# Kernel tuning notes

Hardware: AMD Instinct MI355X
Metric: run time of the kernel (lower is better)

## Reference

```python
import jax, jax.numpy as jnp
import numpy as np

HIDDEN = 512
HEADS = 8
HEAD_DIM = HIDDEN // HEADS


def setup_inputs() -> dict:
    key = jax.random.key(0)
    ks = jax.random.split(key, 12)
    B, S = 2, 2048
    s = 1.0 / np.sqrt(HIDDEN)
    inp = {
        "query": jax.random.normal(ks[0], (B, S, HIDDEN), dtype=jnp.float32),
        "key": jax.random.normal(ks[1], (B, S, HIDDEN), dtype=jnp.float32),
        "value": jax.random.normal(ks[2], (B, S, HIDDEN), dtype=jnp.float32),
        "Wq": jax.random.uniform(ks[3], (HIDDEN, HIDDEN), jnp.float32, -s, s),
        "bq": jnp.zeros((HIDDEN,), jnp.float32),
        "Wk": jax.random.uniform(ks[4], (HIDDEN, HIDDEN), jnp.float32, -s, s),
        "bk": jnp.zeros((HIDDEN,), jnp.float32),
        "Wv": jax.random.uniform(ks[5], (HIDDEN, HIDDEN), jnp.float32, -s, s),
        "bv": jnp.zeros((HIDDEN,), jnp.float32),
        "Wo": jax.random.uniform(ks[6], (HIDDEN, HIDDEN), jnp.float32, -s, s),
        "bo": jnp.zeros((HIDDEN,), jnp.float32),
    }
    return inp


def reference(query, key, value, Wq, bq, Wk, bk, Wv, bv, Wo, bo):
    B, S, _ = query.shape
    scale = jnp.sqrt(jnp.asarray(HEAD_DIM, dtype=query.dtype))
    # Linear projections (torch Linear: x @ W.T + b)
    Q = (query @ Wq.T + bq).reshape(B, S, HEADS, HEAD_DIM).transpose(0, 2, 1, 3)
    K = (key @ Wk.T + bk).reshape(B, S, HEADS, HEAD_DIM).transpose(0, 2, 1, 3)
    V = (value @ Wv.T + bv).reshape(B, S, HEADS, HEAD_DIM).transpose(0, 2, 1, 3)
    # Scores: [B, H, S, S]
    energy = jnp.einsum("bhqd,bhkd->bhqk", Q, K) / scale
    attn = jax.nn.softmax(energy, axis=-1)
    # Dropout is identity in eval mode.
    x = jnp.einsum("bhqk,bhkd->bhqd", attn, V)
    x = x.transpose(0, 2, 1, 3).reshape(B, S, HIDDEN)
    return x @ Wo.T + bo
```

## Files before the change

kernel.cpp:

```cpp
#include <hip/hip_runtime.h>

typedef __bf16 bf16x8 __attribute__((ext_vector_type(8)));
typedef float f32x4 __attribute__((ext_vector_type(4)));
typedef unsigned int uint4v __attribute__((ext_vector_type(4)));
typedef unsigned int uint2v __attribute__((ext_vector_type(2)));

__device__ __forceinline__ unsigned short f2bf(float f) {
  union { float f; unsigned int u; } v; v.f = f;
  unsigned int u = v.u;
  u += 0x7FFFu + ((u >> 16) & 1u);
  return (unsigned short)(u >> 16);
}

__device__ __forceinline__ unsigned int pack2bf(float a, float b) {
  return (unsigned int)f2bf(a) | ((unsigned int)f2bf(b) << 16);
}

__device__ __forceinline__ unsigned int packtrunc(float a, float b) {
  return __builtin_amdgcn_perm(__float_as_uint(b), __float_as_uint(a),
                               0x07060302u);
}

__device__ __forceinline__ bf16x8 as_bf(uint4v u) {
  union { uint4v u; bf16x8 b; } c; c.u = u; return c.b;
}

__global__ __launch_bounds__(256) void convert_w(
    const float* wq, const float* wk, const float* wv, const float* wo,
    unsigned short* wqc, unsigned short* wkc, unsigned short* wvc,
    unsigned short* woc, float qscale)
{
  const float* src; unsigned short* dst; float sc = 1.f;
  switch (blockIdx.y) {
    case 0: src = wq; dst = wqc; sc = qscale; break;
    case 1: src = wk; dst = wkc; break;
    case 2: src = wv; dst = wvc; break;
    default: src = wo; dst = woc; break;
  }
  int idx = (blockIdx.x * 256 + threadIdx.x) * 8;
  f32x4 a = *(const f32x4*)(src + idx);
  f32x4 b = *(const f32x4*)(src + idx + 4);
  uint4v p;
  p.x = pack2bf(a.x * sc, a.y * sc);
  p.y = pack2bf(a.z * sc, a.w * sc);
  p.z = pack2bf(b.x * sc, b.y * sc);
  p.w = pack2bf(b.z * sc, b.w * sc);
  *(uint4v*)(dst + idx) = p;
}

template<int OUT, bool AF32>
__device__ __forceinline__ void gemm_core(
    const void* __restrict__ Ap, const unsigned short* __restrict__ W,
    const float* __restrict__ bias, void* __restrict__ Cp,
    float bscale, int mbase, int nbase)
{
  __shared__ union {
    struct { unsigned short As[2][64][40]; unsigned short Bs[2][128][40]; } t;
    unsigned short Cs[128][72];
  } u;

  const int tid  = threadIdx.x;
  const int wave = tid >> 6, lane = tid & 63;
  const int lrow = lane & 15, lgrp = lane >> 4;
  const int ar = tid >> 2, ac = (tid & 3) * 8;

  const unsigned short* Bg0 = W + (size_t)(nbase + ar) * 512 + ac;
  const unsigned short* Bg1 = W + (size_t)(nbase + ar + 64) * 512 + ac;

  f32x4 acc[4][2];
#pragma unroll
  for (int i = 0; i < 4; i++)
#pragma unroll
    for (int j = 0; j < 2; j++) acc[i][j] = (f32x4){0.f, 0.f, 0.f, 0.f};

  const unsigned short* Ab = (const unsigned short*)Ap;
  const float*          Af = (const float*)Ap;
  uint4v pA; f32x4 pAf0, pAf1;
  if constexpr (AF32) {
    const float* base = Af + (size_t)(mbase + ar) * 512 + ac;
    pAf0 = *(const f32x4*)(base);
    pAf1 = *(const f32x4*)(base + 4);
  } else {
    pA = *(const uint4v*)(Ab + (size_t)(mbase + ar) * 512 + ac);
  }
  uint4v pB0 = *(const uint4v*)Bg0;
  uint4v pB1 = *(const uint4v*)Bg1;

  for (int kt = 0; kt < 512; kt += 32) {
    const int buf = (kt >> 5) & 1;
    if constexpr (AF32) {
      uint4v w;
      w.x = pack2bf(pAf0.x, pAf0.y); w.y = pack2bf(pAf0.z, pAf0.w);
      w.z = pack2bf(pAf1.x, pAf1.y); w.w = pack2bf(pAf1.z, pAf1.w);
      *(uint4v*)&u.t.As[buf][ar][ac] = w;
    } else {
      *(uint4v*)&u.t.As[buf][ar][ac] = pA;
    }
    *(uint4v*)&u.t.Bs[buf][ar][ac]      = pB0;
    *(uint4v*)&u.t.Bs[buf][ar + 64][ac] = pB1;
    if (kt + 32 < 512) {
      if constexpr (AF32) {
        const float* base = Af + (size_t)(mbase + ar) * 512 + ac + kt + 32;
        pAf0 = *(const f32x4*)(base);
        pAf1 = *(const f32x4*)(base + 4);
      } else {
        pA = *(const uint4v*)(Ab + (size_t)(mbase + ar) * 512 + ac + kt + 32);
      }
      pB0 = *(const uint4v*)(Bg0 + kt + 32);
      pB1 = *(const uint4v*)(Bg1 + kt + 32);
    }
    __syncthreads();
    bf16x8 a[4], b[2];
#pragma unroll
    for (int mi = 0; mi < 4; mi++)
      a[mi] = *(const bf16x8*)&u.t.As[buf][mi * 16 + lrow][lgrp * 8];
#pragma unroll
    for (int ni = 0; ni < 2; ni++)
      b[ni] = *(const bf16x8*)&u.t.Bs[buf][wave * 32 + ni * 16 + lrow][lgrp * 8];
#pragma unroll
    for (int mi = 0; mi < 4; mi++)
#pragma unroll
      for (int ni = 0; ni < 2; ni++)
        acc[mi][ni] = __builtin_amdgcn_mfma_f32_16x16x32_bf16(
            a[mi], b[ni], acc[mi][ni], 0, 0, 0);
  }

  if constexpr (OUT == 2) {
    __syncthreads();
#pragma unroll
    for (int ni = 0; ni < 2; ni++) {
      int col_l = wave * 32 + ni * 16 + lrow;
      float bv = bias[nbase + col_l];
#pragma unroll
      for (int mi = 0; mi < 4; mi++) {
        int row_l = mi * 16 + lgrp * 4;
#pragma unroll
        for (int r = 0; r < 4; r++)
          u.Cs[col_l][row_l + r] = f2bf(acc[mi][ni][r] + bv);
      }
    }
    __syncthreads();
    const int bb = mbase >> 11, s_base = mbase & 2047;
    unsigned short* Vt = (unsigned short*)Cp;
#pragma unroll
    for (int ks = 0; ks < 4; ks++) {
      int seg = tid + ks * 256;
      int c = seg >> 3, r0 = (seg & 7) * 8;
      uint4v val = *(const uint4v*)&u.Cs[c][r0];
      int n = nbase + c, hh = n >> 6, d = n & 63;
      int sr = s_base + r0;
      int P0 = (sr & ~31) | (((sr >> 3) & 1) << 4) | (((sr >> 4) & 1) << 2);
      unsigned short* dst = Vt + ((size_t)(bb * 8 + hh) * 64 + d) * 2048;
      *(uint2v*)(dst + P0)     = (uint2v){val.x, val.y};
      *(uint2v*)(dst + P0 + 8) = (uint2v){val.z, val.w};
    }
  } else {
#pragma unroll
    for (int ni = 0; ni < 2; ni++) {
      int col = nbase + wave * 32 + ni * 16 + lrow;
      float bv = bias[col] * bscale;
#pragma unroll
      for (int mi = 0; mi < 4; mi++) {
        int row0 = mbase + mi * 16 + lgrp * 4;
#pragma unroll
        for (int r = 0; r < 4; r++) {
          float val = acc[mi][ni][r] + bv;
          if constexpr (OUT == 0)
            ((unsigned short*)Cp)[(size_t)(row0 + r) * 512 + col] = f2bf(val);
          else
            ((float*)Cp)[(size_t)(row0 + r) * 512 + col] = val;
        }
      }
    }
  }
}

__global__ __launch_bounds__(256) void qkv_gemm(
    const float* q, const float* k, const float* v,
    const unsigned short* wqc, const unsigned short* wkc,
    const unsigned short* wvc,
    const float* bq, const float* bk, const float* bv,
    unsigned short* Qb, unsigned short* Kb, unsigned short* Vt, float qscale)
{
  const int z = blockIdx.z;
  const int mb = blockIdx.y * 64, nb = blockIdx.x * 128;
  if (z == 2)      gemm_core<2, true>(v, wvc, bv, Vt, 1.f, mb, nb);
  else if (z == 0) gemm_core<0, true>(q, wqc, bq, Qb, qscale, mb, nb);
  else             gemm_core<0, true>(k, wkc, bk, Kb, 1.f, mb, nb);
}

__global__ __launch_bounds__(256) void out_gemm(
    const unsigned short* ctx, const unsigned short* woc,
    const float* bo, float* out)
{
  __shared__ unsigned short As[2][64][40];
  __shared__ unsigned short Bs[2][64][40];

  const int tid  = threadIdx.x;
  const int wave = tid >> 6, lane = tid & 63;
  const int lrow = lane & 15, lgrp = lane >> 4;
  const int mbase = blockIdx.y * 64, nbase = blockIdx.x * 64;
  const int ar = tid >> 2, ac = (tid & 3) * 8;

  const unsigned short* Ag = ctx + (size_t)(mbase + ar) * 512 + ac;
  const unsigned short* Bg = woc + (size_t)(nbase + ar) * 512 + ac;

  f32x4 acc[4];
#pragma unroll
  for (int i = 0; i < 4; i++) acc[i] = (f32x4){0.f, 0.f, 0.f, 0.f};

  uint4v pA = *(const uint4v*)Ag;
  uint4v pB = *(const uint4v*)Bg;

  for (int kt = 0; kt < 512; kt += 32) {
    const int buf = (kt >> 5) & 1;
    *(uint4v*)&As[buf][ar][ac] = pA;
    *(uint4v*)&Bs[buf][ar][ac] = pB;
    if (kt + 32 < 512) {
      pA = *(const uint4v*)(Ag + kt + 32);
      pB = *(const uint4v*)(Bg + kt + 32);
    }
    __syncthreads();
    bf16x8 a[4];
#pragma unroll
    for (int mi = 0; mi < 4; mi++)
      a[mi] = *(const bf16x8*)&As[buf][mi * 16 + lrow][lgrp * 8];
    bf16x8 b = *(const bf16x8*)&Bs[buf][wave * 16 + lrow][lgrp * 8];
#pragma unroll
    for (int mi = 0; mi < 4; mi++)
      acc[mi] = __builtin_amdgcn_mfma_f32_16x16x32_bf16(a[mi], b, acc[mi], 0, 0, 0);
  }

  int col = nbase + wave * 16 + lrow;
  float bv = bo[col];
#pragma unroll
  for (int mi = 0; mi < 4; mi++) {
    int row0 = mbase + mi * 16 + lgrp * 4;
#pragma unroll
    for (int r = 0; r < 4; r++)
      out[(size_t)(row0 + r) * 512 + col] = acc[mi][r] + bv;
  }
}

__global__ __launch_bounds__(256, 3) void attn_kernel(
    const unsigned short* Qb, const unsigned short* Kb,
    const unsigned short* Vt, unsigned short* ctx)
{
  __shared__ unsigned short Ks[128][74];
  __shared__ unsigned short Vs[64][134];

  const int tid  = threadIdx.x;
  const int wave = tid >> 6, lane = tid & 63;
  const int lrow = lane & 15, lgrp = lane >> 4;
  const int qh = wave >> 1, kh = wave & 1;
  const int bh = blockIdx.y, b = bh >> 3, h = bh & 7;
  const int qbase = blockIdx.x * 64;

  const unsigned short* Qg  = Qb + (size_t)(b * 2048 + qbase) * 512 + h * 64;
  const unsigned short* Kg  = Kb + (size_t)(b * 2048) * 512 + h * 64;
  const unsigned short* Vtg = Vt + (size_t)bh * 64 * 2048;

#pragma unroll
  for (int i = 0; i < 2; i++) {
    int seg = tid + i * 256;
    int row = seg >> 3, c0 = (seg & 7) * 8;
    *(uint4v*)&Vs[row][c0] = *(const uint4v*)(Qg + (size_t)row * 512 + c0);
  }
  __syncthreads();
  bf16x8 qf[2][2];
#pragma unroll
  for (int qt = 0; qt < 2; qt++)
#pragma unroll
    for (int ks = 0; ks < 2; ks++)
      qf[qt][ks] = *(const bf16x8*)&Vs[qh * 32 + qt * 16 + lrow][ks * 32 + lgrp * 8];

  bf16x8 vone;
  { uint4v o = (uint4v){0x3F803F80u, 0x3F803F80u, 0x3F803F80u, 0x3F803F80u};
    vone = as_bf(o); }

  const int s0  = tid >> 3, kc_ = (tid & 7) * 8;
  const int vd0 = tid >> 4, vc_ = (tid & 15) * 8;

  f32x4 oacc[2][5];
#pragma unroll
  for (int qt = 0; qt < 2; qt++)
#pragma unroll
    for (int d = 0; d < 5; d++) oacc[qt][d] = (f32x4){0.f, 0.f, 0.f, 0.f};

  uint4v kr[4], vr[4];
#pragma unroll
  for (int i = 0; i < 4; i++) {
    kr[i] = *(const uint4v*)(Kg + (size_t)(s0 + 32 * i) * 512 + kc_);
    vr[i] = *(const uint4v*)(Vtg + (size_t)(vd0 + 16 * i) * 2048 + vc_);
  }
  __syncthreads();

  for (int it = 0; it < 16; ++it) {
#pragma unroll
    for (int i = 0; i < 4; i++) {
      *(uint4v*)&Ks[s0 + 32 * i][kc_]  = kr[i];
      *(uint4v*)&Vs[vd0 + 16 * i][vc_] = vr[i];
    }
    __syncthreads();
    if (it < 15) {
      const int key0 = (it + 1) * 128;
#pragma unroll
      for (int i = 0; i < 4; i++) {
        kr[i] = *(const uint4v*)(Kg + (size_t)(key0 + s0 + 32 * i) * 512 + kc_);
        vr[i] = *(const uint4v*)(Vtg + (size_t)(vd0 + 16 * i) * 2048 + key0 + vc_);
      }
    }

    f32x4 sacc[2][4];
#pragma unroll
    for (int qt = 0; qt < 2; qt++)
#pragma unroll
      for (int kt = 0; kt < 4; kt++) sacc[qt][kt] = (f32x4){0.f, 0.f, 0.f, 0.f};
#pragma unroll
    for (int kt = 0; kt < 4; kt++) {
      bf16x8 a0 = *(const bf16x8*)&Ks[kh * 64 + kt * 16 + lrow][lgrp * 8];
      bf16x8 a1 = *(const bf16x8*)&Ks[kh * 64 + kt * 16 + lrow][32 + lgrp * 8];
#pragma unroll
      for (int qt = 0; qt < 2; qt++) {
        sacc[qt][kt] = __builtin_amdgcn_mfma_f32_16x16x32_bf16(a0, qf[qt][0], sacc[qt][kt], 0, 0, 0);
        sacc[qt][kt] = __builtin_amdgcn_mfma_f32_16x16x32_bf16(a1, qf[qt][1], sacc[qt][kt], 0, 0, 0);
      }
    }

#pragma unroll
    for (int qt = 0; qt < 2; qt++)
#pragma unroll
      for (int kt = 0; kt < 4; kt++)
#pragma unroll
        for (int r = 0; r < 4; r++)
          sacc[qt][kt][r] = __builtin_amdgcn_exp2f(sacc[qt][kt][r]);

#pragma unroll
    for (int c = 0; c < 2; c++) {
      bf16x8 pf[2];
#pragma unroll
      for (int qt = 0; qt < 2; qt++) {
        uint4v pk;
        pk.x = packtrunc(sacc[qt][2 * c][0],     sacc[qt][2 * c][1]);
        pk.y = packtrunc(sacc[qt][2 * c][2],     sacc[qt][2 * c][3]);
        pk.z = packtrunc(sacc[qt][2 * c + 1][0], sacc[qt][2 * c + 1][1]);
        pk.w = packtrunc(sacc[qt][2 * c + 1][2], sacc[qt][2 * c + 1][3]);
        pf[qt] = as_bf(pk);
      }
#pragma unroll
      for (int dt = 0; dt < 5; dt++) {
        bf16x8 vb = (dt < 4)
          ? *(const bf16x8*)&Vs[dt * 16 + lrow][(2 * kh + c) * 32 + lgrp * 8]
          : vone;
#pragma unroll
        for (int qt = 0; qt < 2; qt++)
          oacc[qt][dt] = __builtin_amdgcn_mfma_f32_16x16x32_bf16(vb, pf[qt], oacc[qt][dt], 0, 0, 0);
      }
    }
    __syncthreads();
  }

  float* Obuf = (float*)&Ks[0][0];
  float* Lbuf = Obuf + 64 * 68;
  if (kh == 1) {
#pragma unroll
    for (int qt = 0; qt < 2; qt++) {
      int qrow = qh * 32 + qt * 16 + lrow;
#pragma unroll
      for (int dt = 0; dt < 4; dt++)
#pragma unroll
        for (int r = 0; r < 4; r++)
          Obuf[qrow * 68 + dt * 16 + lgrp * 4 + r] = oacc[qt][dt][r];
      if (lgrp == 0) Lbuf[qrow] = oacc[qt][4][0];
    }
  }
  __syncthreads();
  if (kh == 0) {
#pragma unroll
    for (int qt = 0; qt < 2; qt++) {
      int qrow = qh * 32 + qt * 16 + lrow;
      float inv = 1.0f / (oacc[qt][4][0] + Lbuf[qrow]);
#pragma unroll
      for (int dt = 0; dt < 4; dt++)
#pragma unroll
        for (int r = 0; r < 4; r++) {
          float val = (oacc[qt][dt][r] + Obuf[qrow * 68 + dt * 16 + lgrp * 4 + r]) * inv;
          Vs[qrow][dt * 16 + lgrp * 4 + r] = f2bf(val);
        }
    }
  }
  __syncthreads();
  unsigned short* Cg = ctx + (size_t)(b * 2048 + qbase) * 512 + h * 64;
#pragma unroll
  for (int i = 0; i < 2; i++) {
    int seg = tid + i * 256;
    int row = seg >> 3, c0 = (seg & 7) * 8;
    *(uint4v*)(Cg + (size_t)row * 512 + c0) = *(const uint4v*)&Vs[row][c0];
  }
}

extern "C" void kernel_launch(void* const* d_in, const int* in_sizes, int n_in,
                              void* d_out, int out_size, void* d_ws, size_t ws_size,
                              hipStream_t stream)
{
  const float* q  = (const float*)d_in[0];
  const float* k  = (const float*)d_in[1];
  const float* v  = (const float*)d_in[2];
  const float* Wq = (const float*)d_in[3];
  const float* bq = (const float*)d_in[4];
  const float* Wk = (const float*)d_in[5];
  const float* bk = (const float*)d_in[6];
  const float* Wv = (const float*)d_in[7];
  const float* bv = (const float*)d_in[8];
  const float* Wo = (const float*)d_in[9];
  const float* bo = (const float*)d_in[10];
  float* out = (float*)d_out;

  unsigned short* wqc = (unsigned short*)d_ws;
  unsigned short* wkc = wqc + (1 << 18);
  unsigned short* wvc = wkc + (1 << 18);
  unsigned short* woc = wvc + (1 << 18);
  unsigned short* Qb  = woc + (1 << 18);
  unsigned short* Kb  = Qb  + (1 << 21);
  unsigned short* Vt  = Kb  + (1 << 21);
  unsigned short* Cb  = Vt  + (1 << 21);

  const float qscale = 0.125f * 1.44269504088896340736f;

  convert_w<<<dim3(128, 4), 256, 0, stream>>>(
      Wq, Wk, Wv, Wo, wqc, wkc, wvc, woc, qscale);
  qkv_gemm<<<dim3(4, 64, 3), 256, 0, stream>>>(
      q, k, v, wqc, wkc, wvc, bq, bk, bv, Qb, Kb, Vt, qscale);
  attn_kernel<<<dim3(32, 16), 256, 0, stream>>>(Qb, Kb, Vt, Cb);
  out_gemm<<<dim3(8, 64), 256, 0, stream>>>(Cb, woc, bo, out);
}
```

Measured before the change: 144.9 us.

## Widen attention block to 128 queries with 8 waves sharing K/V tiles

The attention kernel now uses 512 threads per block covering 128 query rows instead of 64, so each K/V tile staged in shared memory is reused by twice as many waves and the grid halves. Each thread loads half as many K/V segments per iteration. The shared buffers become a union with a larger fp32 merge area, and the final normalized context is written straight to global memory as packed bf16 pairs instead of going through a shared-memory staging pass. The cost is fewer blocks (256) and lower occupancy bounds, plus narrower, less coalesced output stores.

```diff
diff --git a/kernel.cpp b/kernel.cpp
--- a/kernel.cpp
+++ b/kernel.cpp
@@ -242,19 +242,21 @@
   }
 }
 
-__global__ __launch_bounds__(256, 3) void attn_kernel(
+__global__ __launch_bounds__(512, 2) void attn_kernel(
     const unsigned short* Qb, const unsigned short* Kb,
     const unsigned short* Vt, unsigned short* ctx)
 {
-  __shared__ unsigned short Ks[128][74];
-  __shared__ unsigned short Vs[64][134];
+  __shared__ union {
+    struct { unsigned short Ks[128][74]; unsigned short Vs[64][134]; } s;
+    struct { float O[128][68]; float L[128]; } m;
+  } u;
 
   const int tid  = threadIdx.x;
   const int wave = tid >> 6, lane = tid & 63;
   const int lrow = lane & 15, lgrp = lane >> 4;
   const int qh = wave >> 1, kh = wave & 1;
   const int bh = blockIdx.y, b = bh >> 3, h = bh & 7;
-  const int qbase = blockIdx.x * 64;
+  const int qbase = blockIdx.x * 128;
 
   const unsigned short* Qg  = Qb + (size_t)(b * 2048 + qbase) * 512 + h * 64;
   const unsigned short* Kg  = Kb + (size_t)(b * 2048) * 512 + h * 64;
@@ -262,9 +264,9 @@
 
 #pragma unroll
   for (int i = 0; i < 2; i++) {
-    int seg = tid + i * 256;
+    int seg = tid + i * 512;
     int row = seg >> 3, c0 = (seg & 7) * 8;
-    *(uint4v*)&Vs[row][c0] = *(const uint4v*)(Qg + (size_t)row * 512 + c0);
+    *(uint4v*)&u.s.Ks[row][c0] = *(const uint4v*)(Qg + (size_t)row * 512 + c0);
   }
   __syncthreads();
   bf16x8 qf[2][2];
@@ -272,7 +274,7 @@
   for (int qt = 0; qt < 2; qt++)
 #pragma unroll
     for (int ks = 0; ks < 2; ks++)
-      qf[qt][ks] = *(const bf16x8*)&Vs[qh * 32 + qt * 16 + lrow][ks * 32 + lgrp * 8];
+      qf[qt][ks] = *(const bf16x8*)&u.s.Ks[qh * 32 + qt * 16 + lrow][ks * 32 + lgrp * 8];
 
   bf16x8 vone;
   { uint4v o = (uint4v){0x3F803F80u, 0x3F803F80u, 0x3F803F80u, 0x3F803F80u};
@@ -287,27 +289,27 @@
 #pragma unroll
     for (int d = 0; d < 5; d++) oacc[qt][d] = (f32x4){0.f, 0.f, 0.f, 0.f};
 
-  uint4v kr[4], vr[4];
-#pragma unroll
-  for (int i = 0; i < 4; i++) {
-    kr[i] = *(const uint4v*)(Kg + (size_t)(s0 + 32 * i) * 512 + kc_);
-    vr[i] = *(const uint4v*)(Vtg + (size_t)(vd0 + 16 * i) * 2048 + vc_);
+  uint4v kr[2], vr[2];
+#pragma unroll
+  for (int i = 0; i < 2; i++) {
+    kr[i] = *(const uint4v*)(Kg + (size_t)(s0 + 64 * i) * 512 + kc_);
+    vr[i] = *(const uint4v*)(Vtg + (size_t)(vd0 + 32 * i) * 2048 + vc_);
   }
   __syncthreads();
 
   for (int it = 0; it < 16; ++it) {
 #pragma unroll
-    for (int i = 0; i < 4; i++) {
-      *(uint4v*)&Ks[s0 + 32 * i][kc_]  = kr[i];
-      *(uint4v*)&Vs[vd0 + 16 * i][vc_] = vr[i];
+    for (int i = 0; i < 2; i++) {
+      *(uint4v*)&u.s.Ks[s0 + 64 * i][kc_]  = kr[i];
+      *(uint4v*)&u.s.Vs[vd0 + 32 * i][vc_] = vr[i];
     }
     __syncthreads();
     if (it < 15) {
       const int key0 = (it + 1) * 128;
 #pragma unroll
-      for (int i = 0; i < 4; i++) {
-        kr[i] = *(const uint4v*)(Kg + (size_t)(key0 + s0 + 32 * i) * 512 + kc_);
-        vr[i] = *(const uint4v*)(Vtg + (size_t)(vd0 + 16 * i) * 2048 + key0 + vc_);
+      for (int i = 0; i < 2; i++) {
+        kr[i] = *(const uint4v*)(Kg + (size_t)(key0 + s0 + 64 * i) * 512 + kc_);
+        vr[i] = *(const uint4v*)(Vtg + (size_t)(vd0 + 32 * i) * 2048 + key0 + vc_);
       }
     }
 
@@ -318,8 +320,8 @@
       for (int kt = 0; kt < 4; kt++) sacc[qt][kt] = (f32x4){0.f, 0.f, 0.f, 0.f};
 #pragma unroll
     for (int kt = 0; kt < 4; kt++) {
-      bf16x8 a0 = *(const bf16x8*)&Ks[kh * 64 + kt * 16 + lrow][lgrp * 8];
-      bf16x8 a1 = *(const bf16x8*)&Ks[kh * 64 + kt * 16 + lrow][32 + lgrp * 8];
+      bf16x8 a0 = *(const bf16x8*)&u.s.Ks[kh * 64 + kt * 16 + lrow][lgrp * 8];
+      bf16x8 a1 = *(const bf16x8*)&u.s.Ks[kh * 64 + kt * 16 + lrow][32 + lgrp * 8];
 #pragma unroll
       for (int qt = 0; qt < 2; qt++) {
         sacc[qt][kt] = __builtin_amdgcn_mfma_f32_16x16x32_bf16(a0, qf[qt][0], sacc[qt][kt], 0, 0, 0);
@@ -350,7 +352,7 @@
 #pragma unroll
       for (int dt = 0; dt < 5; dt++) {
         bf16x8 vb = (dt < 4)
-          ? *(const bf16x8*)&Vs[dt * 16 + lrow][(2 * kh + c) * 32 + lgrp * 8]
+          ? *(const bf16x8*)&u.s.Vs[dt * 16 + lrow][(2 * kh + c) * 32 + lgrp * 8]
           : vone;
 #pragma unroll
         for (int qt = 0; qt < 2; qt++)
@@ -360,8 +362,6 @@
     __syncthreads();
   }
 
-  float* Obuf = (float*)&Ks[0][0];
-  float* Lbuf = Obuf + 64 * 68;
   if (kh == 1) {
 #pragma unroll
     for (int qt = 0; qt < 2; qt++) {
@@ -370,32 +370,29 @@
       for (int dt = 0; dt < 4; dt++)
 #pragma unroll
         for (int r = 0; r < 4; r++)
-          Obuf[qrow * 68 + dt * 16 + lgrp * 4 + r] = oacc[qt][dt][r];
-      if (lgrp == 0) Lbuf[qrow] = oacc[qt][4][0];
+          u.m.O[qrow][dt * 16 + lgrp * 4 + r] = oacc[qt][dt][r];
+      if (lgrp == 0) u.m.L[qrow] = oacc[qt][4][0];
     }
   }
   __syncthreads();
   if (kh == 0) {
+    unsigned short* Cg = ctx + (size_t)(b * 2048 + qbase) * 512 + h * 64;
 #pragma unroll
     for (int qt = 0; qt < 2; qt++) {
       int qrow = qh * 32 + qt * 16 + lrow;
-      float inv = 1.0f / (oacc[qt][4][0] + Lbuf[qrow]);
-#pragma unroll
-      for (int dt = 0; dt < 4; dt++)
-#pragma unroll
-        for (int r = 0; r < 4; r++) {
-          float val = (oacc[qt][dt][r] + Obuf[qrow * 68 + dt * 16 + lgrp * 4 + r]) * inv;
-          Vs[qrow][dt * 16 + lgrp * 4 + r] = f2bf(val);
-        }
-    }
-  }
-  __syncthreads();
-  unsigned short* Cg = ctx + (size_t)(b * 2048 + qbase) * 512 + h * 64;
-#pragma unroll
-  for (int i = 0; i < 2; i++) {
-    int seg = tid + i * 256;
-    int row = seg >> 3, c0 = (seg & 7) * 8;
-    *(uint4v*)(Cg + (size_t)row * 512 + c0) = *(const uint4v*)&Vs[row][c0];
+      float inv = 1.0f / (oacc[qt][4][0] + u.m.L[qrow]);
+#pragma unroll
+      for (int dt = 0; dt < 4; dt++) {
+        float v0 = (oacc[qt][dt][0] + u.m.O[qrow][dt * 16 + lgrp * 4 + 0]) * inv;
+        float v1 = (oacc[qt][dt][1] + u.m.O[qrow][dt * 16 + lgrp * 4 + 1]) * inv;
+        float v2 = (oacc[qt][dt][2] + u.m.O[qrow][dt * 16 + lgrp * 4 + 2]) * inv;
+        float v3 = (oacc[qt][dt][3] + u.m.O[qrow][dt * 16 + lgrp * 4 + 3]) * inv;
+        uint2v pk;
+        pk.x = pack2bf(v0, v1);
+        pk.y = pack2bf(v2, v3);
+        *(uint2v*)(Cg + (size_t)qrow * 512 + dt * 16 + lgrp * 4) = pk;
+      }
+    }
   }
 }
 
@@ -431,6 +428,6 @@
       Wq, Wk, Wv, Wo, wqc, wkc, wvc, woc, qscale);
   qkv_gemm<<<dim3(4, 64, 3), 256, 0, stream>>>(
       q, k, v, wqc, wkc, wvc, bq, bk, bv, Qb, Kb, Vt, qscale);
-  attn_kernel<<<dim3(32, 16), 256, 0, stream>>>(Qb, Kb, Vt, Cb);
+  attn_kernel<<<dim3(16, 16), 512, 0, stream>>>(Qb, Kb, Vt, Cb);
   out_gemm<<<dim3(8, 64), 256, 0, stream>>>(Cb, woc, bo, out);
 }
```

After: 145.5 us. About the same (+0.4%).
